# Kernel optimization log

Measured on AMD Instinct MI355X. Metric: run time of the kernel, lower is better.

Reference implementation:

```python
import jax, jax.numpy as jnp
import numpy as np

NEG = -1000000000.0

def setup_inputs() -> dict:
    key = jax.random.key(0)
    k1, k2, k3, k4 = jax.random.split(key, 4)
    B, S, D = 8, 4096, 256
    query = jax.random.normal(k1, (B, S, D), dtype=jnp.float32)
    k_ = jax.random.normal(k2, (B, S, D), dtype=jnp.float32)
    value = jax.random.normal(k3, (B, S, D), dtype=jnp.float32)
    mask = jax.random.bernoulli(k4, 0.1, (B, S, 1))  # True = masked
    return {"query": query, "key": k_, "value": value, "mask": mask}

def reference(query, key, value, mask):
    # a: [B,S,1] sum of squares of query; b: [B,S,1] for key
    a = jnp.sum(query * query, axis=-1, keepdims=True)
    b = jnp.sum(key * key, axis=-1, keepdims=True)
    # s1 = (K^T / b) @ V  -> [B, D, D]; divide each key row s by b_s
    s1 = jnp.einsum('bsd,bse->bde', key / b, value)
    # score = Q / a, masked rows set to -1e9
    score = query / a
    score = jnp.where(mask, NEG, score)
    s2 = jnp.einsum('bsd,bde->bse', score, s1)
    return s2 / query.shape[-1]
```

## Files before the change

kernel.cpp:

```cpp
#include <hip/hip_runtime.h>

#define BB 8
#define SS 4096
#define DD 256
#define NEGV -1000000000.0f
#define NCH (SS / 32)

typedef float f32x4 __attribute__((ext_vector_type(4)));
typedef short s16x8 __attribute__((ext_vector_type(8)));

static __device__ __forceinline__ unsigned short f2bf(float x) {
  unsigned int u = __builtin_bit_cast(unsigned int, x);
  u += 0x7fffu + ((u >> 16) & 1u);
  return (unsigned short)(u >> 16);
}

static __device__ __forceinline__ void gload_lds16(
    const unsigned short* __restrict__ g, unsigned short* l) {
  __builtin_amdgcn_global_load_lds(
      (const __attribute__((address_space(1))) void*)g,
      (__attribute__((address_space(3))) void*)l, 16, 0, 0);
}

__global__ __launch_bounds__(256, 4) void prep_kernel(
    const float* __restrict__ Q, const float* __restrict__ K,
    const float* __restrict__ V, const int* __restrict__ mask,
    unsigned short* __restrict__ QS, unsigned short* __restrict__ KT,
    unsigned short* __restrict__ VT) {
  __shared__ unsigned short tile[32 * 260];
  const int b = blockIdx.y;
  const int sc = blockIdx.x;
  const int s0 = sc * 32;
  const int tid = threadIdx.x;
  const int w = tid >> 6, l = tid & 63;

  if (blockIdx.z == 0) {
    float4 reg[8];
    float ps[8];
#pragma unroll
    for (int it = 0; it < 8; ++it) {
      const int row = it * 4 + w;
      reg[it] = *(const float4*)(Q + ((size_t)b * SS + s0 + row) * DD + l * 4);
    }
    int mk[8];
#pragma unroll
    for (int it = 0; it < 8; ++it) mk[it] = mask[b * SS + s0 + it * 4 + w];
#pragma unroll
    for (int it = 0; it < 8; ++it)
      ps[it] = reg[it].x * reg[it].x + reg[it].y * reg[it].y +
               reg[it].z * reg[it].z + reg[it].w * reg[it].w;
#pragma unroll
    for (int off = 32; off; off >>= 1)
#pragma unroll
      for (int it = 0; it < 8; ++it) ps[it] += __shfl_xor(ps[it], off);
#pragma unroll
    for (int it = 0; it < 8; ++it) {
      const int row = it * 4 + w;
      const float ca = mk[it] ? 0.0f : (1.0f / ps[it]);
      const float aa = mk[it] ? NEGV : 0.0f;
      ushort4 o;
      o.x = f2bf(reg[it].x * ca + aa);
      o.y = f2bf(reg[it].y * ca + aa);
      o.z = f2bf(reg[it].z * ca + aa);
      o.w = f2bf(reg[it].w * ca + aa);
      *(ushort4*)(QS + ((size_t)b * SS + s0 + row) * DD + l * 4) = o;
    }
    return;
  }

  const int isK = (blockIdx.z == 1);
  const float* __restrict__ src = isK ? K : V;
  unsigned short* __restrict__ dst = isK ? KT : VT;

  float4 reg[8];
  float ps[8];
#pragma unroll
  for (int it = 0; it < 8; ++it) {
    const int row = it * 4 + w;
    reg[it] = *(const float4*)(src + ((size_t)b * SS + s0 + row) * DD + l * 4);
  }
#pragma unroll
  for (int it = 0; it < 8; ++it)
    ps[it] = reg[it].x * reg[it].x + reg[it].y * reg[it].y +
             reg[it].z * reg[it].z + reg[it].w * reg[it].w;
  float scl[8];
  if (isK) {
#pragma unroll
    for (int off = 32; off; off >>= 1)
#pragma unroll
      for (int it = 0; it < 8; ++it) ps[it] += __shfl_xor(ps[it], off);
#pragma unroll
    for (int it = 0; it < 8; ++it) scl[it] = 1.0f / ps[it];
  } else {
#pragma unroll
    for (int it = 0; it < 8; ++it) scl[it] = 1.0f;
  }
#pragma unroll
  for (int it = 0; it < 8; ++it) {
    const int row = it * 4 + w;
    ushort4 o;
    o.x = f2bf(reg[it].x * scl[it]);
    o.y = f2bf(reg[it].y * scl[it]);
    o.z = f2bf(reg[it].z * scl[it]);
    o.w = f2bf(reg[it].w * scl[it]);
    *(ushort4*)(tile + row * 260 + l * 4) = o;
  }
  __syncthreads();
  const size_t gbase = ((size_t)(b * NCH + sc) * DD + tid) * 32;
#pragma unroll
  for (int c = 0; c < 4; ++c) {
    union { unsigned short h[8]; uint4 v; } u;
#pragma unroll
    for (int j = 0; j < 8; ++j) u.h[j] = tile[(c * 8 + j) * 260 + tid];
    *(uint4*)(dst + gbase + c * 8) = u.v;
  }
}

__global__ __launch_bounds__(256) void p2_kernel(
    const unsigned short* __restrict__ KT, const unsigned short* __restrict__ VT,
    float* __restrict__ part, int iters) {
  __shared__ unsigned short vt_l[2][128 * 32];
  __shared__ unsigned short kt_l[2][128 * 32];
  const int b = blockIdx.z;
  const int d0 = (blockIdx.x & 1) * 128;
  const int e0 = (blockIdx.x >> 1) * 128;
  const int tid = threadIdx.x;
  const int w = tid >> 6, l = tid & 63;
  const int wr = w & 1, wc = w >> 1;
  const int quad = l >> 4, mr = l & 15;

  f32x4 acc[4][4];
#pragma unroll
  for (int i = 0; i < 4; ++i)
#pragma unroll
    for (int j = 0; j < 4; ++j) acc[i][j] = (f32x4){0.f, 0.f, 0.f, 0.f};

  for (int ks = 0; ks < iters; ++ks) {
    const int c0 = (blockIdx.y * iters + ks) * 2;
#pragma unroll
    for (int h = 0; h < 2; ++h) {
      const size_t vch = ((size_t)(b * NCH + c0 + h) * DD + e0) * 32 + l * 8;
      const size_t kch = ((size_t)(b * NCH + c0 + h) * DD + d0) * 32 + l * 8;
#pragma unroll
      for (int g = 0; g < 2; ++g) {
        const int r0 = w * 32 + g * 16;
        gload_lds16(VT + vch + (size_t)r0 * 32, &vt_l[h][r0 * 32]);
        gload_lds16(KT + kch + (size_t)r0 * 32, &kt_l[h][r0 * 32]);
      }
    }
    __syncthreads();
#pragma unroll
    for (int kh = 0; kh < 2; ++kh) {
      s16x8 af[4], bfr[4];
#pragma unroll
      for (int i = 0; i < 4; ++i)
        af[i] = *(const s16x8*)(&vt_l[kh][(wr * 64 + i * 16 + mr) * 32 + quad * 8]);
#pragma unroll
      for (int j = 0; j < 4; ++j)
        bfr[j] = *(const s16x8*)(&kt_l[kh][(wc * 64 + j * 16 + mr) * 32 + quad * 8]);
#pragma unroll
      for (int i = 0; i < 4; ++i)
#pragma unroll
        for (int j = 0; j < 4; ++j)
          acc[i][j] = __builtin_amdgcn_mfma_f32_16x16x32_bf16(af[i], bfr[j],
                                                              acc[i][j], 0, 0, 0);
    }
    __syncthreads();
  }

  float* pb = part + ((size_t)blockIdx.y * BB + b) * DD * DD;
#pragma unroll
  for (int i = 0; i < 4; ++i) {
    const int e = e0 + wr * 64 + i * 16 + quad * 4;
#pragma unroll
    for (int j = 0; j < 4; ++j) {
      const int d = d0 + wc * 64 + j * 16 + mr;
      float* p = pb + (size_t)e * DD + d;
#pragma unroll
      for (int r = 0; r < 4; ++r) p[(size_t)r * DD] = acc[i][j][r];
    }
  }
}

__global__ __launch_bounds__(256) void reduce_kernel(
    const float* __restrict__ part, unsigned short* __restrict__ s1b,
    int split) {
  const size_t i4 = ((size_t)blockIdx.x * 256 + threadIdx.x) * 4;
  float ax = 0.f, ay = 0.f, az = 0.f, aw = 0.f;
  for (int p = 0; p < split; ++p) {
    const float4 v = *(const float4*)(part + (size_t)p * (BB * DD * DD) + i4);
    ax += v.x; ay += v.y; az += v.z; aw += v.w;
  }
  ushort4 o;
  o.x = f2bf(ax); o.y = f2bf(ay); o.z = f2bf(az); o.w = f2bf(aw);
  *(ushort4*)(s1b + i4) = o;
}

__global__ __launch_bounds__(256) void p3_kernel(
    const unsigned short* __restrict__ QS, const unsigned short* __restrict__ s1b,
    float* __restrict__ out) {
  __shared__ unsigned short qs_l[2][128 * 32];
  __shared__ unsigned short s1_l[2][128 * 32];
  const int b = blockIdx.z;
  const int e0 = blockIdx.x * 128;
  const int s0 = blockIdx.y * 128;
  const int tid = threadIdx.x;
  const int w = tid >> 6, l = tid & 63;
  const int wr = w & 1, wc = w >> 1;
  const int quad = l >> 4, mr = l & 15;
  const int lr = l >> 2;
  const int lc = (l & 3) * 8;

  f32x4 acc[4][4];
#pragma unroll
  for (int i = 0; i < 4; ++i)
#pragma unroll
    for (int j = 0; j < 4; ++j) acc[i][j] = (f32x4){0.f, 0.f, 0.f, 0.f};

  for (int ks = 0; ks < 4; ++ks) {
    const int dc = ks * 64;
#pragma unroll
    for (int h = 0; h < 2; ++h)
#pragma unroll
      for (int g = 0; g < 2; ++g) {
        const int r0 = w * 32 + g * 16;
        gload_lds16(QS + ((size_t)b * SS + s0 + r0 + lr) * DD + dc + h * 32 + lc,
                    &qs_l[h][r0 * 32]);
        gload_lds16(s1b + ((size_t)b * DD + e0 + r0 + lr) * DD + dc + h * 32 + lc,
                    &s1_l[h][r0 * 32]);
      }
    __syncthreads();
#pragma unroll
    for (int kh = 0; kh < 2; ++kh) {
      s16x8 af[4], bfr[4];
#pragma unroll
      for (int i = 0; i < 4; ++i)
        af[i] = *(const s16x8*)(&qs_l[kh][(wr * 64 + i * 16 + mr) * 32 + quad * 8]);
#pragma unroll
      for (int j = 0; j < 4; ++j)
        bfr[j] = *(const s16x8*)(&s1_l[kh][(wc * 64 + j * 16 + mr) * 32 + quad * 8]);
#pragma unroll
      for (int i = 0; i < 4; ++i)
#pragma unroll
        for (int j = 0; j < 4; ++j)
          acc[i][j] = __builtin_amdgcn_mfma_f32_16x16x32_bf16(af[i], bfr[j],
                                                              acc[i][j], 0, 0, 0);
    }
    __syncthreads();
  }

#pragma unroll
  for (int i = 0; i < 4; ++i) {
    const int s = s0 + wr * 64 + i * 16 + quad * 4;
#pragma unroll
    for (int j = 0; j < 4; ++j) {
      const int e = e0 + wc * 64 + j * 16 + mr;
      float* p = out + ((size_t)b * SS + s) * DD + e;
#pragma unroll
      for (int r = 0; r < 4; ++r) p[(size_t)r * DD] = acc[i][j][r] * (1.0f / DD);
    }
  }
}

extern "C" void kernel_launch(void* const* d_in, const int* in_sizes, int n_in,
                              void* d_out, int out_size, void* d_ws,
                              size_t ws_size, hipStream_t stream) {
  const float* Q = (const float*)d_in[0];
  const float* K = (const float*)d_in[1];
  const float* V = (const float*)d_in[2];
  const int* mask = (const int*)d_in[3];
  float* out = (float*)d_out;

  char* ws = (char*)d_ws;
  const size_t MB = (size_t)1024 * 1024;
  unsigned short* QS = (unsigned short*)(ws);
  unsigned short* KT = (unsigned short*)(ws + 16 * MB);
  unsigned short* VT = (unsigned short*)(ws + 32 * MB);
  float* part = (float*)(ws + 48 * MB);

  const int split = (ws_size >= (size_t)82 * MB) ? 16 : 8;
  const int iters = SS / (64 * split);
  unsigned short* s1b =
      (unsigned short*)(ws + 48 * MB + (size_t)split * 2 * MB);

  prep_kernel<<<dim3(SS / 32, BB, 3), 256, 0, stream>>>(Q, K, V, mask, QS, KT,
                                                        VT);
  p2_kernel<<<dim3(4, split, BB), 256, 0, stream>>>(KT, VT, part, iters);
  reduce_kernel<<<dim3(512), 256, 0, stream>>>(part, s1b, split);
  p3_kernel<<<dim3(2, SS / 128, BB), 256, 0, stream>>>(QS, s1b, out);
}
```

Measured before the change: 171.6 us.

## Double-buffer LDS tiles in both GEMM kernels and pin prep load scheduling

```diff
diff --git a/kernel.cpp b/kernel.cpp
--- a/kernel.cpp
+++ b/kernel.cpp
@@ -37,14 +37,15 @@
   if (blockIdx.z == 0) {
     float4 reg[8];
     float ps[8];
+    int mk[8];
 #pragma unroll
     for (int it = 0; it < 8; ++it) {
       const int row = it * 4 + w;
       reg[it] = *(const float4*)(Q + ((size_t)b * SS + s0 + row) * DD + l * 4);
     }
-    int mk[8];
 #pragma unroll
     for (int it = 0; it < 8; ++it) mk[it] = mask[b * SS + s0 + it * 4 + w];
+    __builtin_amdgcn_sched_barrier(0);
 #pragma unroll
     for (int it = 0; it < 8; ++it)
       ps[it] = reg[it].x * reg[it].x + reg[it].y * reg[it].y +
@@ -79,6 +80,7 @@
     const int row = it * 4 + w;
     reg[it] = *(const float4*)(src + ((size_t)b * SS + s0 + row) * DD + l * 4);
   }
+  __builtin_amdgcn_sched_barrier(0);
 #pragma unroll
   for (int it = 0; it < 8; ++it)
     ps[it] = reg[it].x * reg[it].x + reg[it].y * reg[it].y +
@@ -119,8 +121,8 @@
 __global__ __launch_bounds__(256) void p2_kernel(
     const unsigned short* __restrict__ KT, const unsigned short* __restrict__ VT,
     float* __restrict__ part, int iters) {
-  __shared__ unsigned short vt_l[2][128 * 32];
-  __shared__ unsigned short kt_l[2][128 * 32];
+  __shared__ unsigned short vt_l[2][2][128 * 32];
+  __shared__ unsigned short kt_l[2][2][128 * 32];
   const int b = blockIdx.z;
   const int d0 = (blockIdx.x & 1) * 128;
   const int e0 = (blockIdx.x >> 1) * 128;
@@ -135,7 +137,7 @@
 #pragma unroll
     for (int j = 0; j < 4; ++j) acc[i][j] = (f32x4){0.f, 0.f, 0.f, 0.f};
 
-  for (int ks = 0; ks < iters; ++ks) {
+  auto stage = [&](int buf, int ks) {
     const int c0 = (blockIdx.y * iters + ks) * 2;
 #pragma unroll
     for (int h = 0; h < 2; ++h) {
@@ -144,20 +146,26 @@
 #pragma unroll
       for (int g = 0; g < 2; ++g) {
         const int r0 = w * 32 + g * 16;
-        gload_lds16(VT + vch + (size_t)r0 * 32, &vt_l[h][r0 * 32]);
-        gload_lds16(KT + kch + (size_t)r0 * 32, &kt_l[h][r0 * 32]);
+        gload_lds16(VT + vch + (size_t)r0 * 32, &vt_l[buf][h][r0 * 32]);
+        gload_lds16(KT + kch + (size_t)r0 * 32, &kt_l[buf][h][r0 * 32]);
       }
     }
-    __syncthreads();
+  };
+
+  stage(0, 0);
+  __syncthreads();
+  int cur = 0;
+  for (int ks = 0; ks < iters; ++ks) {
+    if (ks + 1 < iters) stage(cur ^ 1, ks + 1);
 #pragma unroll
     for (int kh = 0; kh < 2; ++kh) {
       s16x8 af[4], bfr[4];
 #pragma unroll
       for (int i = 0; i < 4; ++i)
-        af[i] = *(const s16x8*)(&vt_l[kh][(wr * 64 + i * 16 + mr) * 32 + quad * 8]);
+        af[i] = *(const s16x8*)(&vt_l[cur][kh][(wr * 64 + i * 16 + mr) * 32 + quad * 8]);
 #pragma unroll
       for (int j = 0; j < 4; ++j)
-        bfr[j] = *(const s16x8*)(&kt_l[kh][(wc * 64 + j * 16 + mr) * 32 + quad * 8]);
+        bfr[j] = *(const s16x8*)(&kt_l[cur][kh][(wc * 64 + j * 16 + mr) * 32 + quad * 8]);
 #pragma unroll
       for (int i = 0; i < 4; ++i)
 #pragma unroll
@@ -166,6 +174,7 @@
                                                               acc[i][j], 0, 0, 0);
     }
     __syncthreads();
+    cur ^= 1;
   }
 
   float* pb = part + ((size_t)blockIdx.y * BB + b) * DD * DD;
@@ -199,8 +208,8 @@
 __global__ __launch_bounds__(256) void p3_kernel(
     const unsigned short* __restrict__ QS, const unsigned short* __restrict__ s1b,
     float* __restrict__ out) {
-  __shared__ unsigned short qs_l[2][128 * 32];
-  __shared__ unsigned short s1_l[2][128 * 32];
+  __shared__ unsigned short qs_l[2][2][128 * 32];
+  __shared__ unsigned short s1_l[2][2][128 * 32];
   const int b = blockIdx.z;
   const int e0 = blockIdx.x * 128;
   const int s0 = blockIdx.y * 128;
@@ -217,7 +226,7 @@
 #pragma unroll
     for (int j = 0; j < 4; ++j) acc[i][j] = (f32x4){0.f, 0.f, 0.f, 0.f};
 
-  for (int ks = 0; ks < 4; ++ks) {
+  auto stage = [&](int buf, int ks) {
     const int dc = ks * 64;
 #pragma unroll
     for (int h = 0; h < 2; ++h)
@@ -225,20 +234,26 @@
       for (int g = 0; g < 2; ++g) {
         const int r0 = w * 32 + g * 16;
         gload_lds16(QS + ((size_t)b * SS + s0 + r0 + lr) * DD + dc + h * 32 + lc,
-                    &qs_l[h][r0 * 32]);
+                    &qs_l[buf][h][r0 * 32]);
         gload_lds16(s1b + ((size_t)b * DD + e0 + r0 + lr) * DD + dc + h * 32 + lc,
-                    &s1_l[h][r0 * 32]);
+                    &s1_l[buf][h][r0 * 32]);
       }
-    __syncthreads();
+  };
+
+  stage(0, 0);
+  __syncthreads();
+  int cur = 0;
+  for (int ks = 0; ks < 4; ++ks) {
+    if (ks + 1 < 4) stage(cur ^ 1, ks + 1);
 #pragma unroll
     for (int kh = 0; kh < 2; ++kh) {
       s16x8 af[4], bfr[4];
 #pragma unroll
       for (int i = 0; i < 4; ++i)
-        af[i] = *(const s16x8*)(&qs_l[kh][(wr * 64 + i * 16 + mr) * 32 + quad * 8]);
+        af[i] = *(const s16x8*)(&qs_l[cur][kh][(wr * 64 + i * 16 + mr) * 32 + quad * 8]);
 #pragma unroll
       for (int j = 0; j < 4; ++j)
-        bfr[j] = *(const s16x8*)(&s1_l[kh][(wc * 64 + j * 16 + mr) * 32 + quad * 8]);
+        bfr[j] = *(const s16x8*)(&s1_l[cur][kh][(wc * 64 + j * 16 + mr) * 32 + quad * 8]);
 #pragma unroll
       for (int i = 0; i < 4; ++i)
 #pragma unroll
@@ -247,6 +262,7 @@
                                                               acc[i][j], 0, 0, 0);
     }
     __syncthreads();
+    cur ^= 1;
   }
 
 #pragma unroll
```

Measured after the change: 174.3 us. About the same (+1.6%).

## Fuse query normalization into output GEMM and store split-K partials as bf16

Applied to the files above, without the earlier changes.

```diff
diff --git a/kernel.cpp b/kernel.cpp
--- a/kernel.cpp
+++ b/kernel.cpp
@@ -5,6 +5,7 @@
 #define DD 256
 #define NEGV -1000000000.0f
 #define NCH (SS / 32)
+#define SPLIT 16
 
 typedef float f32x4 __attribute__((ext_vector_type(4)));
 typedef short s16x8 __attribute__((ext_vector_type(8)));
@@ -13,6 +14,9 @@
   unsigned int u = __builtin_bit_cast(unsigned int, x);
   u += 0x7fffu + ((u >> 16) & 1u);
   return (unsigned short)(u >> 16);
+}
+static __device__ __forceinline__ float bf2f(unsigned short h) {
+  return __builtin_bit_cast(float, (unsigned int)h << 16);
 }
 
 static __device__ __forceinline__ void gload_lds16(
@@ -23,52 +27,15 @@
 }
 
 __global__ __launch_bounds__(256, 4) void prep_kernel(
-    const float* __restrict__ Q, const float* __restrict__ K,
-    const float* __restrict__ V, const int* __restrict__ mask,
-    unsigned short* __restrict__ QS, unsigned short* __restrict__ KT,
-    unsigned short* __restrict__ VT) {
+    const float* __restrict__ K, const float* __restrict__ V,
+    unsigned short* __restrict__ KT, unsigned short* __restrict__ VT) {
   __shared__ unsigned short tile[32 * 260];
   const int b = blockIdx.y;
   const int sc = blockIdx.x;
   const int s0 = sc * 32;
   const int tid = threadIdx.x;
   const int w = tid >> 6, l = tid & 63;
-
-  if (blockIdx.z == 0) {
-    float4 reg[8];
-    float ps[8];
-#pragma unroll
-    for (int it = 0; it < 8; ++it) {
-      const int row = it * 4 + w;
-      reg[it] = *(const float4*)(Q + ((size_t)b * SS + s0 + row) * DD + l * 4);
-    }
-    int mk[8];
-#pragma unroll
-    for (int it = 0; it < 8; ++it) mk[it] = mask[b * SS + s0 + it * 4 + w];
-#pragma unroll
-    for (int it = 0; it < 8; ++it)
-      ps[it] = reg[it].x * reg[it].x + reg[it].y * reg[it].y +
-               reg[it].z * reg[it].z + reg[it].w * reg[it].w;
-#pragma unroll
-    for (int off = 32; off; off >>= 1)
-#pragma unroll
-      for (int it = 0; it < 8; ++it) ps[it] += __shfl_xor(ps[it], off);
-#pragma unroll
-    for (int it = 0; it < 8; ++it) {
-      const int row = it * 4 + w;
-      const float ca = mk[it] ? 0.0f : (1.0f / ps[it]);
-      const float aa = mk[it] ? NEGV : 0.0f;
-      ushort4 o;
-      o.x = f2bf(reg[it].x * ca + aa);
-      o.y = f2bf(reg[it].y * ca + aa);
-      o.z = f2bf(reg[it].z * ca + aa);
-      o.w = f2bf(reg[it].w * ca + aa);
-      *(ushort4*)(QS + ((size_t)b * SS + s0 + row) * DD + l * 4) = o;
-    }
-    return;
-  }
-
-  const int isK = (blockIdx.z == 1);
+  const int isK = (blockIdx.z == 0);
   const float* __restrict__ src = isK ? K : V;
   unsigned short* __restrict__ dst = isK ? KT : VT;
 
@@ -118,7 +85,7 @@
 
 __global__ __launch_bounds__(256) void p2_kernel(
     const unsigned short* __restrict__ KT, const unsigned short* __restrict__ VT,
-    float* __restrict__ part, int iters) {
+    unsigned short* __restrict__ part, int iters) {
   __shared__ unsigned short vt_l[2][128 * 32];
   __shared__ unsigned short kt_l[2][128 * 32];
   const int b = blockIdx.z;
@@ -168,39 +135,60 @@
     __syncthreads();
   }
 
-  float* pb = part + ((size_t)blockIdx.y * BB + b) * DD * DD;
+  unsigned short* pb = part + ((size_t)blockIdx.y * BB + b) * DD * DD;
 #pragma unroll
   for (int i = 0; i < 4; ++i) {
     const int e = e0 + wr * 64 + i * 16 + quad * 4;
 #pragma unroll
     for (int j = 0; j < 4; ++j) {
       const int d = d0 + wc * 64 + j * 16 + mr;
-      float* p = pb + (size_t)e * DD + d;
-#pragma unroll
-      for (int r = 0; r < 4; ++r) p[(size_t)r * DD] = acc[i][j][r];
+      unsigned short* p = pb + (size_t)e * DD + d;
+#pragma unroll
+      for (int r = 0; r < 4; ++r) p[(size_t)r * DD] = f2bf(acc[i][j][r]);
     }
   }
 }
 
 __global__ __launch_bounds__(256) void reduce_kernel(
-    const float* __restrict__ part, unsigned short* __restrict__ s1b,
-    int split) {
-  const size_t i4 = ((size_t)blockIdx.x * 256 + threadIdx.x) * 4;
-  float ax = 0.f, ay = 0.f, az = 0.f, aw = 0.f;
-  for (int p = 0; p < split; ++p) {
-    const float4 v = *(const float4*)(part + (size_t)p * (BB * DD * DD) + i4);
-    ax += v.x; ay += v.y; az += v.z; aw += v.w;
-  }
-  ushort4 o;
-  o.x = f2bf(ax); o.y = f2bf(ay); o.z = f2bf(az); o.w = f2bf(aw);
-  *(ushort4*)(s1b + i4) = o;
+    const unsigned short* __restrict__ part, unsigned short* __restrict__ s1b,
+    float* __restrict__ colsum) {
+  const int tid = threadIdx.x;
+  const size_t i8 = ((size_t)blockIdx.x * 256 + tid) * 8;
+  float a[8];
+#pragma unroll
+  for (int j = 0; j < 8; ++j) a[j] = 0.f;
+  for (int p = 0; p < SPLIT; ++p) {
+    union { uint4 v; unsigned short h[8]; } u;
+    u.v = *(const uint4*)(part + (size_t)p * (BB * DD * DD) + i8);
+#pragma unroll
+    for (int j = 0; j < 8; ++j) a[j] += bf2f(u.h[j]);
+  }
+  union { uint4 v; unsigned short h[8]; } o;
+#pragma unroll
+  for (int j = 0; j < 8; ++j) o.h[j] = f2bf(a[j]);
+  *(uint4*)(s1b + i8) = o.v;
+  float rp = (a[0] + a[1]) + (a[2] + a[3]) + ((a[4] + a[5]) + (a[6] + a[7]));
+  rp += __shfl_xor(rp, 1);
+  rp += __shfl_xor(rp, 2);
+  rp += __shfl_xor(rp, 4);
+  rp += __shfl_xor(rp, 8);
+  rp += __shfl_xor(rp, 16);
+  if ((tid & 31) == 0) {
+    const int e = (int)((i8 >> 8) & 255);
+    const int bb = (int)(i8 >> 16);
+    colsum[bb * DD + e] = rp;
+  }
 }
 
 __global__ __launch_bounds__(256) void p3_kernel(
-    const unsigned short* __restrict__ QS, const unsigned short* __restrict__ s1b,
+    const float* __restrict__ Q, const int* __restrict__ mask,
+    const unsigned short* __restrict__ s1b, const float* __restrict__ colsum,
     float* __restrict__ out) {
-  __shared__ unsigned short qs_l[2][128 * 32];
+  __shared__ unsigned short qs_l[2][128 * 32 + 16];
   __shared__ unsigned short s1_l[2][128 * 32];
+  __shared__ float ps_l[128];
+  __shared__ float ca_l[128];
+  __shared__ float cs_l[128];
   const int b = blockIdx.z;
   const int e0 = blockIdx.x * 128;
   const int s0 = blockIdx.y * 128;
@@ -210,12 +198,19 @@
   const int quad = l >> 4, mr = l & 15;
   const int lr = l >> 2;
   const int lc = (l & 3) * 8;
+  const int rg = tid >> 4;
+  const int c4 = tid & 15;
+
+  if (tid < 128) cs_l[tid] = colsum[b * DD + e0 + tid];
 
   f32x4 acc[4][4];
 #pragma unroll
   for (int i = 0; i < 4; ++i)
 #pragma unroll
     for (int j = 0; j < 4; ++j) acc[i][j] = (f32x4){0.f, 0.f, 0.f, 0.f};
+  float np[8];
+#pragma unroll
+  for (int u = 0; u < 8; ++u) np[u] = 0.f;
 
   for (int ks = 0; ks < 4; ++ks) {
     const int dc = ks * 64;
@@ -224,11 +219,24 @@
 #pragma unroll
       for (int g = 0; g < 2; ++g) {
         const int r0 = w * 32 + g * 16;
-        gload_lds16(QS + ((size_t)b * SS + s0 + r0 + lr) * DD + dc + h * 32 + lc,
-                    &qs_l[h][r0 * 32]);
         gload_lds16(s1b + ((size_t)b * DD + e0 + r0 + lr) * DD + dc + h * 32 + lc,
                     &s1_l[h][r0 * 32]);
       }
+    float4 qv[8];
+#pragma unroll
+    for (int u = 0; u < 8; ++u) {
+      const int row = rg + u * 16;
+      qv[u] = *(const float4*)(Q + ((size_t)b * SS + s0 + row) * DD + dc + c4 * 4);
+    }
+#pragma unroll
+    for (int u = 0; u < 8; ++u) {
+      np[u] += qv[u].x * qv[u].x + qv[u].y * qv[u].y + qv[u].z * qv[u].z +
+               qv[u].w * qv[u].w;
+      ushort4 o;
+      o.x = f2bf(qv[u].x); o.y = f2bf(qv[u].y);
+      o.z = f2bf(qv[u].z); o.w = f2bf(qv[u].w);
+      *(ushort4*)&qs_l[c4 >> 3][(rg + u * 16) * 32 + (c4 & 7) * 4] = o;
+    }
     __syncthreads();
 #pragma unroll
     for (int kh = 0; kh < 2; ++kh) {
@@ -250,14 +258,37 @@
   }
 
 #pragma unroll
+  for (int u = 0; u < 8; ++u) {
+    np[u] += __shfl_xor(np[u], 1);
+    np[u] += __shfl_xor(np[u], 2);
+    np[u] += __shfl_xor(np[u], 4);
+    np[u] += __shfl_xor(np[u], 8);
+  }
+  if (c4 == 0) {
+#pragma unroll
+    for (int u = 0; u < 8; ++u) ps_l[rg + u * 16] = np[u];
+  }
+  __syncthreads();
+  if (tid < 128) {
+    const int mk = mask[b * SS + s0 + tid];
+    ca_l[tid] = mk ? 0.0f : (1.0f / ps_l[tid]);
+  }
+  __syncthreads();
+
+#pragma unroll
   for (int i = 0; i < 4; ++i) {
-    const int s = s0 + wr * 64 + i * 16 + quad * 4;
 #pragma unroll
     for (int j = 0; j < 4; ++j) {
-      const int e = e0 + wc * 64 + j * 16 + mr;
-      float* p = out + ((size_t)b * SS + s) * DD + e;
-#pragma unroll
-      for (int r = 0; r < 4; ++r) p[(size_t)r * DD] = acc[i][j][r] * (1.0f / DD);
+      const int el = wc * 64 + j * 16 + mr;
+      const float csum = cs_l[el];
+      float* p = out + ((size_t)b * SS + s0 + wr * 64 + i * 16 + quad * 4) * DD +
+                 e0 + el;
+#pragma unroll
+      for (int r = 0; r < 4; ++r) {
+        const float ca = ca_l[wr * 64 + i * 16 + quad * 4 + r];
+        const float val = (ca != 0.0f) ? acc[i][j][r] * ca : NEGV * csum;
+        p[(size_t)r * DD] = val * (1.0f / DD);
+      }
     }
   }
 }
@@ -273,19 +304,18 @@
 
   char* ws = (char*)d_ws;
   const size_t MB = (size_t)1024 * 1024;
-  unsigned short* QS = (unsigned short*)(ws);
-  unsigned short* KT = (unsigned short*)(ws + 16 * MB);
-  unsigned short* VT = (unsigned short*)(ws + 32 * MB);
-  float* part = (float*)(ws + 48 * MB);
-
-  const int split = (ws_size >= (size_t)82 * MB) ? 16 : 8;
-  const int iters = SS / (64 * split);
-  unsigned short* s1b =
-      (unsigned short*)(ws + 48 * MB + (size_t)split * 2 * MB);
-
-  prep_kernel<<<dim3(SS / 32, BB, 3), 256, 0, stream>>>(Q, K, V, mask, QS, KT,
-                                                        VT);
-  p2_kernel<<<dim3(4, split, BB), 256, 0, stream>>>(KT, VT, part, iters);
-  reduce_kernel<<<dim3(512), 256, 0, stream>>>(part, s1b, split);
-  p3_kernel<<<dim3(2, SS / 128, BB), 256, 0, stream>>>(QS, s1b, out);
-}
+  unsigned short* KT = (unsigned short*)(ws);
+  unsigned short* VT = (unsigned short*)(ws + 16 * MB);
+  unsigned short* part = (unsigned short*)(ws + 32 * MB);
+  unsigned short* s1b = (unsigned short*)(ws + 48 * MB);
+  float* colsum = (float*)(ws + 49 * MB);
+
+  const int iters = SS / (64 * SPLIT);
+
+  prep_kernel<<<dim3(SS / 32, BB, 2), 256, 0, stream>>>(K, V, KT, VT);
+  p2_kernel<<<dim3(4, SPLIT, BB), 256, 0, stream>>>(KT, VT, part, iters);
+  reduce_kernel<<<dim3(BB * DD * DD / (8 * 256)), 256, 0, stream>>>(part, s1b,
+                                                                    colsum);
+  p3_kernel<<<dim3(2, SS / 128, BB), 256, 0, stream>>>(Q, mask, s1b, colsum,
+                                                       out);
+}
```

After: 170.0 us. Within noise of the previous version (-0.9%).
